# Performance work log

Hardware: AMD Instinct MI355X
Metric: run time of the kernel (lower is better)

## Reference

```python
import jax, jax.numpy as jnp
import numpy as np

DIM = 4096
N_HEADS = 32
HEAD_DIM = DIM // N_HEADS  # 128
BSZ = 2
SEQLEN = 2048


def setup_inputs() -> dict:
    key = jax.random.key(0)
    ks = jax.random.split(key, 8)
    x = jax.random.normal(ks[0], (BSZ, SEQLEN, DIM), dtype=jnp.float32)
    # rotary frequencies (LLaMA): theta = 10000^{-2i/d}, angle = pos * theta
    inv_freq = 1.0 / (10000.0 ** (np.arange(0, HEAD_DIM, 2, dtype=np.float32) / HEAD_DIM))
    angles = np.arange(SEQLEN, dtype=np.float32)[:, None] * inv_freq[None, :]  # [S, hd/2]
    freqs_cos = jnp.asarray(np.cos(angles))
    freqs_sin = jnp.asarray(np.sin(angles))
    # causal additive mask [1,1,S,S]
    neg = jnp.float32(-1e9)
    mask = jnp.where(jnp.tril(jnp.ones((SEQLEN, SEQLEN), dtype=bool)), 0.0, neg)[None, None]
    scale = 0.02
    wq = jax.random.normal(ks[1], (DIM, DIM), dtype=jnp.float32) * scale
    wk = jax.random.normal(ks[2], (DIM, DIM), dtype=jnp.float32) * scale
    wv = jax.random.normal(ks[3], (DIM, DIM), dtype=jnp.float32) * scale
    wo = jax.random.normal(ks[4], (DIM, DIM), dtype=jnp.float32) * scale
    return {"x": x, "start_pos": 0, "freqs_cos": freqs_cos, "freqs_sin": freqs_sin,
            "mask": mask, "wq": wq, "wk": wk, "wv": wv, "wo": wo}


def _apply_rotary(t, cos, sin):
    # t: [B,S,H,hd]; cos/sin: [S,hd/2] -> broadcast [1,S,1,hd/2]
    t = t.reshape(*t.shape[:-1], HEAD_DIM // 2, 2)
    t0, t1 = t[..., 0], t[..., 1]
    c = cos[None, :, None, :]
    s = sin[None, :, None, :]
    r0 = t0 * c - t1 * s
    r1 = t0 * s + t1 * c
    return jnp.stack([r0, r1], axis=-1).reshape(*t0.shape[:-1], HEAD_DIM)


def reference(x, start_pos, freqs_cos, freqs_sin, mask, wq, wk, wv, wo):
    bsz, seqlen, _ = x.shape
    # QKV projections (nn.Linear: y = x @ W.T; weights stored [out,in])
    xq = (x @ wq.T).reshape(bsz, seqlen, N_HEADS, HEAD_DIM)
    xk = (x @ wk.T).reshape(bsz, seqlen, N_HEADS, HEAD_DIM)
    xv = (x @ wv.T).reshape(bsz, seqlen, N_HEADS, HEAD_DIM)
    xq = _apply_rotary(xq, freqs_cos, freqs_sin)
    xk = _apply_rotary(xk, freqs_cos, freqs_sin)
    # [B,H,S,hd]
    q = xq.transpose(0, 2, 1, 3)
    k = xk.transpose(0, 2, 1, 3)
    v = xv.transpose(0, 2, 1, 3)
    scale = 1.0 / jnp.sqrt(jnp.float32(HEAD_DIM))
    scores = jnp.einsum('bhqd,bhkd->bhqk', q, k) * scale + mask
    probs = jax.nn.softmax(scores, axis=-1)
    out = jnp.einsum('bhqk,bhkd->bhqd', probs, v)  # [B,H,S,hd]
    out = out.transpose(0, 2, 1, 3).reshape(bsz, seqlen, DIM)
    return out @ wo.T
```

## Files before the change

kernel.cpp:

```cpp
#include <hip/hip_runtime.h>

typedef unsigned short ushort_t;
typedef unsigned int u32;
typedef short bf16x8 __attribute__((ext_vector_type(8)));
typedef float f32x4 __attribute__((ext_vector_type(4)));
typedef float f32x16 __attribute__((ext_vector_type(16)));
typedef u32 u32x4 __attribute__((ext_vector_type(4)));

__device__ __forceinline__ ushort_t f2bf(float f) {
  u32 u = __builtin_bit_cast(u32, f);
  u += 0x7FFFu + ((u >> 16) & 1u);
  return (ushort_t)(u >> 16);
}
__device__ __forceinline__ float bf2f(u32 bits16) {
  return __builtin_bit_cast(float, bits16 << 16);
}

__device__ __forceinline__ void cvt_body(const float* __restrict__ in,
                                         ushort_t* __restrict__ out, int i) {
  const float4 a = ((const float4*)in)[(size_t)i * 2];
  const float4 b = ((const float4*)in)[(size_t)i * 2 + 1];
  uint4 r;
  r.x = (u32)f2bf(a.x) | ((u32)f2bf(a.y) << 16);
  r.y = (u32)f2bf(a.z) | ((u32)f2bf(a.w) << 16);
  r.z = (u32)f2bf(b.x) | ((u32)f2bf(b.y) << 16);
  r.w = (u32)f2bf(b.z) | ((u32)f2bf(b.w) << 16);
  ((uint4*)out)[i] = r;
}

__device__ __forceinline__ void cvt_perm_body(const float* __restrict__ in,
                                              ushort_t* __restrict__ out, int i) {
  const int row = i >> 9, k8 = i & 511;
  const int q = row & 31;
  const int lrow = (row & ~31) | ((q < 16) ? (2 * q) : (2 * (q - 16) + 1));
  const float4 a = ((const float4*)in)[(size_t)lrow * 1024 + k8 * 2];
  const float4 b = ((const float4*)in)[(size_t)lrow * 1024 + k8 * 2 + 1];
  uint4 r;
  r.x = (u32)f2bf(a.x) | ((u32)f2bf(a.y) << 16);
  r.y = (u32)f2bf(a.z) | ((u32)f2bf(a.w) << 16);
  r.z = (u32)f2bf(b.x) | ((u32)f2bf(b.y) << 16);
  r.w = (u32)f2bf(b.z) | ((u32)f2bf(b.w) << 16);
  ((uint4*)out)[(size_t)row * 512 + k8] = r;
}

__global__ __launch_bounds__(256)
void cvt_kernel(const float* __restrict__ in, ushort_t* __restrict__ out) {
  cvt_body(in, out, blockIdx.x * 256 + threadIdx.x);
}

__global__ __launch_bounds__(256)
void cvt_perm_kernel(const float* __restrict__ in, ushort_t* __restrict__ out) {
  cvt_perm_body(in, out, blockIdx.x * 256 + threadIdx.x);
}

__global__ __launch_bounds__(256)
void cvt2_kernel(const float* __restrict__ i0, ushort_t* __restrict__ o0,
                 const float* __restrict__ i1, ushort_t* __restrict__ o1,
                 const float* __restrict__ fcos, const float* __restrict__ fsin,
                 float2* __restrict__ cst) {
  const int i = blockIdx.x * 256 + threadIdx.x;
  if (blockIdx.y == 0) {
    if (blockIdx.x < 512) cst[i] = make_float2(fcos[i], fsin[i]);
    cvt_body(i0, o0, i);
  } else {
    cvt_perm_body(i1, o1, i);
  }
}

template <int F32OUT, int ROPE>
__global__ __launch_bounds__(512, 2)
void gemm256(const ushort_t* __restrict__ A, const ushort_t* __restrict__ B,
             void* __restrict__ C, const float2* __restrict__ cst, float qsc) {
  constexpr int KD = 4096, ND = 4096;
  __shared__ ushort_t sA[2][2][128 * 64];
  __shared__ ushort_t sB[2][2][128 * 64];
  const int tid = threadIdx.x;
  const int lane = tid & 63, wave = tid >> 6;
  const int lq = lane & 15, g = lane >> 4;
  const int wm = wave >> 2, wn = wave & 3;
  const int id = blockIdx.x;
  const int swz = (id & 7) * 32 + (id >> 3);
  const int bm = (swz >> 4) * 256;
  const int bn = (swz & 15) * 256;
  const int csw = ((lane & 7) ^ (lane >> 3)) * 8;
  const int srow = lane >> 3;

  f32x4 acc[8][4];
#pragma unroll
  for (int m = 0; m < 8; ++m)
#pragma unroll
    for (int n = 0; n < 4; ++n) acc[m][n] = (f32x4)0.f;

#define STG(sbuf, G, rowb, t_, s_, h_)                                               \
  {                                                                                  \
    _Pragma("unroll") for (int i_ = 0; i_ < 2; ++i_) {                               \
      const int r0_ = wave * 16 + i_ * 8;                                            \
      const int tc_ = (t_) > 63 ? 63 : (t_);                                         \
      const ushort_t* src_ =                                                         \
          (G) + (size_t)((rowb) + (h_) * 128 + r0_ + srow) * KD + tc_ * 64 + csw;    \
      __builtin_amdgcn_global_load_lds(                                              \
          (const __attribute__((address_space(1))) u32*)src_,                        \
          (__attribute__((address_space(3))) u32*)&sbuf[s_][h_][r0_ * 64 + lane * 8],\
          16, 0, 0);                                                                 \
    }                                                                                \
  }
#define RD_A(S_, H_, mf_, kk_)                                                        \
  (*(const bf16x8*)&sA[S_][H_][(wm * 64 + (mf_) * 16 + lq) * 64 +                     \
                               ((((kk_) * 4 + g) ^ (lq & 7)) * 8)])
#define RD_B(S_, H_, nf_, kk_)                                                        \
  (*(const bf16x8*)&sB[S_][H_][(wn * 32 + (nf_) * 16 + lq) * 64 +                     \
                               ((((kk_) * 4 + g) ^ (lq & 7)) * 8)])
#define MM2(MB, B0R, B1R)                                                             \
  _Pragma("unroll") for (int mf = 0; mf < 4; ++mf)                                    \
    _Pragma("unroll") for (int nf = 0; nf < 2; ++nf)                                  \
      _Pragma("unroll") for (int kk = 0; kk < 2; ++kk) {                              \
        acc[(MB) + mf][nf] = __builtin_amdgcn_mfma_f32_16x16x32_bf16(                 \
            af[mf][kk], B0R[nf][kk], acc[(MB) + mf][nf], 0, 0, 0);                    \
        acc[(MB) + mf][2 + nf] = __builtin_amdgcn_mfma_f32_16x16x32_bf16(             \
            af[mf][kk], B1R[nf][kk], acc[(MB) + mf][2 + nf], 0, 0, 0);                \
      }

  STG(sA, A, bm, 0, 0, 0); STG(sA, A, bm, 0, 0, 1);
  STG(sB, B, bn, 0, 0, 0); STG(sB, B, bn, 0, 0, 1);
  asm volatile("s_waitcnt vmcnt(0)" ::: "memory");
  __builtin_amdgcn_s_barrier();
  __builtin_amdgcn_sched_barrier(0);

  bf16x8 af[4][2], b0[2][2], b1[2][2];

#define TILE(S_, T_)                                                                  \
  STG(sA, A, bm, (T_) + 1, (S_) ^ 1, 0);                                              \
  STG(sA, A, bm, (T_) + 1, (S_) ^ 1, 1);                                              \
  STG(sB, B, bn, (T_) + 1, (S_) ^ 1, 0);                                              \
  STG(sB, B, bn, (T_) + 1, (S_) ^ 1, 1);                                              \
  _Pragma("unroll") for (int mf = 0; mf < 4; ++mf)                                    \
    _Pragma("unroll") for (int kk = 0; kk < 2; ++kk)                                  \
      af[mf][kk] = RD_A(S_, 0, mf, kk);                                               \
  _Pragma("unroll") for (int nf = 0; nf < 2; ++nf)                                    \
    _Pragma("unroll") for (int kk = 0; kk < 2; ++kk) {                                \
      b0[nf][kk] = RD_B(S_, 0, nf, kk);                                               \
      b1[nf][kk] = RD_B(S_, 1, nf, kk);                                               \
    }                                                                                 \
  __builtin_amdgcn_s_setprio(1);                                                      \
  MM2(0, b0, b1);                                                                     \
  __builtin_amdgcn_s_setprio(0);                                                      \
  _Pragma("unroll") for (int mf = 0; mf < 4; ++mf)                                    \
    _Pragma("unroll") for (int kk = 0; kk < 2; ++kk)                                  \
      af[mf][kk] = RD_A(S_, 1, mf, kk);                                               \
  __builtin_amdgcn_s_setprio(1);                                                      \
  MM2(4, b0, b1);                                                                     \
  __builtin_amdgcn_s_setprio(0);                                                      \
  asm volatile("s_waitcnt vmcnt(0)" ::: "memory");                                    \
  __builtin_amdgcn_s_barrier();                                                       \
  __builtin_amdgcn_sched_barrier(0);

  for (int t = 0; t < 64; t += 2) {
    TILE(0, t)
    TILE(1, t + 1)
  }
#undef TILE
#undef STG
#undef RD_A
#undef RD_B
#undef MM2

  if (ROPE) {
    const int p = wn * 16 + lq;
#pragma unroll
    for (int m = 0; m < 8; ++m) {
      const int grow = bm + (m >> 2) * 128 + wm * 64 + (m & 3) * 16 + g * 4;
#pragma unroll
      for (int r = 0; r < 4; ++r) {
        const int row = grow + r;
        const float2 cs = cst[(size_t)(row & 2047) * 64 + p];
#pragma unroll
        for (int pr = 0; pr < 2; ++pr) {
          const float t0 = acc[m][pr * 2][r];
          const float t1 = acc[m][pr * 2 + 1][r];
          const int c0 = bn + pr * 128 + wn * 32 + lq;
          ((ushort_t*)C)[(size_t)row * ND + c0] =
              f2bf((t0 * cs.x - t1 * cs.y) * qsc);
          ((ushort_t*)C)[(size_t)row * ND + c0 + 16] =
              f2bf((t0 * cs.y + t1 * cs.x) * qsc);
        }
      }
    }
  } else {
#pragma unroll
    for (int m = 0; m < 8; ++m) {
      const int grow = bm + (m >> 2) * 128 + wm * 64 + (m & 3) * 16 + g * 4;
#pragma unroll
      for (int r = 0; r < 4; ++r) {
        const int row = grow + r;
#pragma unroll
        for (int n = 0; n < 4; ++n) {
          const int gcol = bn + (n >> 1) * 128 + wn * 32 + (n & 1) * 16 + lq;
          if (F32OUT)
            ((float*)C)[(size_t)row * ND + gcol] = acc[m][n][r];
          else
            ((ushort_t*)C)[(size_t)row * ND + gcol] = f2bf(acc[m][n][r]);
        }
      }
    }
  }
}

__global__ __launch_bounds__(256, 2)
void attn_kernel(const ushort_t* __restrict__ Q, const ushort_t* __restrict__ K,
                 const ushort_t* __restrict__ Vt, ushort_t* __restrict__ O) {
  __shared__ ushort_t sK[2][32 * 128];
  __shared__ ushort_t sV[2][128 * 32];
  __shared__ float sScr[4][32];

  const int lane = threadIdx.x & 63, wave = threadIdx.x >> 6;
  const int lq = lane & 31, hi = lane >> 5;
  const int bp = blockIdx.x;
  const int bh = bp >> 3, j = bp & 7;
  const int h = bh & 31, b = bh >> 5;
  const ushort_t* Kb_ = K + (size_t)(b * 2048) * 4096 + h * 128;
  const ushort_t* Vb_ = Vt + (size_t)(h * 128) * 4096 + b * 2048;

#define STAGE(buf, kt_)                                                              \
  {                                                                                  \
    const int kb_ = (kt_) * 32;                                                      \
    _Pragma("unroll")                                                                \
    for (int i_ = 0; i_ < 2; ++i_) {                                                 \
      const int c_ = wave + i_ * 4;                                                  \
      const int krow = c_ * 4 + (lane >> 4);                                         \
      const int kcol = (lane & 15) ^ (krow & 7);                                     \
      const ushort_t* ksrc = Kb_ + (size_t)(kb_ + krow) * 4096 + kcol * 8;           \
      __builtin_amdgcn_global_load_lds(                                              \
          (const __attribute__((address_space(1))) u32*)ksrc,                        \
          (__attribute__((address_space(3))) u32*)&sK[buf][c_ * 512 + lane * 8],     \
          16, 0, 0);                                                                 \
      const int sst = c_ * 64 + lane;                                                \
      const int dv = sst >> 2;                                                       \
      const int gl = (sst & 3) ^ ((sst >> 3) & 3);                                   \
      const ushort_t* vsrc = Vb_ + (size_t)dv * 4096 + kb_ + gl * 8;                 \
      __builtin_amdgcn_global_load_lds(                                              \
          (const __attribute__((address_space(1))) u32*)vsrc,                        \
          (__attribute__((address_space(3))) u32*)&sV[buf][sst * 8], 16, 0, 0);      \
    }                                                                                \
  }

  for (int ph = 0; ph < 2; ++ph) {
    const int qj = ph ? (15 - j) : j;
    const int qbase = qj * 128 + wave * 32;
    const int ntw = qj * 4 + wave + 1;
    const int ntmax = qj * 4 + 4;

    bf16x8 aq[8];
    const ushort_t* qrow = Q + (size_t)(b * 2048 + qbase + lq) * 4096 + h * 128 + hi * 8;
#pragma unroll
    for (int kf = 0; kf < 8; ++kf) aq[kf] = *(const bf16x8*)(qrow + kf * 16);

    f32x16 o[4];
#pragma unroll
    for (int dt = 0; dt < 4; ++dt) o[dt] = (f32x16)0.f;
    float m_run = -1e30f, l_run = 0.f;

    int cur = 0;
    STAGE(0, 0);
    __syncthreads();

    for (int kt = 0; kt < ntmax; ++kt) {
      if (kt + 1 < ntmax) STAGE(cur ^ 1, kt + 1);
      if (kt < ntw) {
        const int kb = kt * 32;
        f32x16 st = (f32x16)0.f;
#pragma unroll
        for (int kf = 0; kf < 8; ++kf) {
          const bf16x8 kfrag =
              *(const bf16x8*)&sK[cur][lq * 128 + (((kf * 2 + hi) ^ (lq & 7)) * 8)];
          st = __builtin_amdgcn_mfma_f32_32x32x16_bf16(kfrag, aq[kf], st, 0, 0, 0);
        }
        if (kt == ntw - 1) {
          const int q = qbase + lq;
#pragma unroll
          for (int r = 0; r < 16; ++r) {
            const int key = kb + (r & 3) + 8 * (r >> 2) + 4 * hi;
            if (key > q) st[r] = -1e30f;
          }
        }
        float tm = st[0];
#pragma unroll
        for (int r = 1; r < 16; ++r) tm = fmaxf(tm, st[r]);
        tm = fmaxf(tm, __shfl_xor(tm, 32));
        if (!__all(tm <= m_run + 8.f)) {
          const float mnew = fmaxf(m_run, tm);
          const float corr = __expf(m_run - mnew);
          m_run = mnew;
          l_run *= corr;
          if (hi == 0) sScr[wave][lq] = corr;
          float fr[16];
#pragma unroll
          for (int r = 0; r < 16; ++r)
            fr[r] = sScr[wave][(r & 3) + 8 * (r >> 2) + 4 * hi];
#pragma unroll
          for (int dt = 0; dt < 4; ++dt)
#pragma unroll
            for (int r = 0; r < 16; ++r) o[dt][r] *= fr[r];
        }
        float rs = 0.f;
#pragma unroll
        for (int r = 0; r < 16; ++r) { st[r] = __expf(st[r] - m_run); rs += st[r]; }
        rs += __shfl_xor(rs, 32);
        l_run += rs;
        u32 A_, B_, C_, D_, E_, F_, G_, H_;
#define CVTPK(d_, l_, h_) \
  asm("v_cvt_pk_bf16_f32 %0, %1, %2" : "=v"(d_) : "v"(l_), "v"(h_))
        CVTPK(A_, st[0], st[1]);  CVTPK(B_, st[4], st[5]);
        CVTPK(C_, st[2], st[3]);  CVTPK(D_, st[6], st[7]);
        CVTPK(E_, st[8], st[9]);  CVTPK(F_, st[12], st[13]);
        CVTPK(G_, st[10], st[11]); CVTPK(H_, st[14], st[15]);
#undef CVTPK
        asm volatile("v_permlane32_swap_b32 %0, %1" : "+v"(A_), "+v"(B_));
        asm volatile("v_permlane32_swap_b32 %0, %1" : "+v"(C_), "+v"(D_));
        asm volatile("v_permlane32_swap_b32 %0, %1" : "+v"(E_), "+v"(F_));
        asm volatile("v_permlane32_swap_b32 %0, %1" : "+v"(G_), "+v"(H_));
        const bf16x8 pa0 = __builtin_bit_cast(bf16x8, (u32x4){A_, C_, B_, D_});
        const bf16x8 pa1 = __builtin_bit_cast(bf16x8, (u32x4){E_, G_, F_, H_});
#pragma unroll
        for (int dt = 0; dt < 4; ++dt) {
          const int d0 = dt * 32 + lq;
          const int s0 = 4 * d0 + ((hi + 0) ^ ((d0 >> 1) & 3));
          const int s1 = 4 * d0 + ((hi + 2) ^ ((d0 >> 1) & 3));
          const bf16x8 vf0 = *(const bf16x8*)&sV[cur][s0 * 8];
          const bf16x8 vf1 = *(const bf16x8*)&sV[cur][s1 * 8];
          o[dt] = __builtin_amdgcn_mfma_f32_32x32x16_bf16(pa0, vf0, o[dt], 0, 0, 0);
          o[dt] = __builtin_amdgcn_mfma_f32_32x32x16_bf16(pa1, vf1, o[dt], 0, 0, 0);
        }
      }
      __syncthreads();
      cur ^= 1;
    }

    if (hi == 0) sScr[wave][lq] = 1.f / l_run;
    __syncthreads();
    const size_t obase = (size_t)(b * 2048 + qbase) * 4096 + h * 128;
#pragma unroll
    for (int r = 0; r < 16; ++r) {
      const int qr = (r & 3) + 8 * (r >> 2) + 4 * hi;
      const float f = sScr[wave][qr];
#pragma unroll
      for (int dt = 0; dt < 4; ++dt)
        O[obase + (size_t)qr * 4096 + dt * 32 + lq] = f2bf(o[dt][r] * f);
    }
    __syncthreads();
  }
#undef STAGE
}

extern "C" void kernel_launch(void* const* d_in, const int* in_sizes, int n_in,
                              void* d_out, int out_size, void* d_ws, size_t ws_size,
                              hipStream_t stream) {
  const float* x = (const float*)d_in[0];
  const float* fcos = (const float*)d_in[2];
  const float* fsin = (const float*)d_in[3];
  const float* wq = (const float*)d_in[5];
  const float* wk = (const float*)d_in[6];
  const float* wv = (const float*)d_in[7];
  const float* wo = (const float*)d_in[8];
  float* out = (float*)d_out;
  char* ws = (char*)d_ws;
  const size_t MB32 = 33554432;
  ushort_t* xb = (ushort_t*)(ws);
  ushort_t* wb = (ushort_t*)(ws + MB32);
  ushort_t* Qb = (ushort_t*)(ws + 2 * MB32);
  ushort_t* Kb = (ushort_t*)(ws + 3 * MB32);
  ushort_t* Vt = (ushort_t*)(ws + 4 * MB32);
  ushort_t* Ob = xb;
  float2* cst = (float2*)d_out;

  const dim3 cb(256);
  const dim3 cg(8192);
  const dim3 gb(512);
  const dim3 gg(256);
  const float QSC = 0.08838834764831845f;

  hipLaunchKernelGGL(cvt2_kernel, dim3(8192, 2), cb, 0, stream, x, xb, wq, wb,
                     fcos, fsin, cst);
  hipLaunchKernelGGL((gemm256<0, 1>), gg, gb, 0, stream, xb, wb, (void*)Qb, cst, QSC);
  hipLaunchKernelGGL(cvt_perm_kernel, cg, cb, 0, stream, wk, wb);
  hipLaunchKernelGGL((gemm256<0, 1>), gg, gb, 0, stream, xb, wb, (void*)Kb, cst, 1.f);
  hipLaunchKernelGGL(cvt_kernel, cg, cb, 0, stream, wv, wb);
  hipLaunchKernelGGL((gemm256<0, 0>), gg, gb, 0, stream, wb, xb, (void*)Vt, cst, 1.f);
  hipLaunchKernelGGL(attn_kernel, dim3(512), cb, 0, stream, Qb, Kb, Vt, Ob);
  hipLaunchKernelGGL(cvt_kernel, cg, cb, 0, stream, wo, wb);
  hipLaunchKernelGGL((gemm256<1, 0>), gg, gb, 0, stream, Ob, wb, (void*)out, cst, 1.f);
}
```

Before: 664.9 us.

## Restructure GEMM mainloop into quadrant-staged pipeline with deeper prefetch

The GEMM main loop drops the two-stage pattern, where each iteration issues all loads for the next tile and then waits on vmcnt(0). It now splits work into four MFMA quadrants, each paired with its own LDS reads and global-to-LDS loads, and prefetches half-tiles two steps ahead with a partial vmcnt(6) wait. The goal is to hide global-load latency behind MFMA work and avoid the full drain at every tile. In exchange it adds many more workgroup barriers per tile, and the buffer-reuse ordering is intricate, so it risks LDS hazards and barrier stalls.

```diff
diff --git a/kernel.cpp b/kernel.cpp
--- a/kernel.cpp
+++ b/kernel.cpp
@@ -110,49 +110,64 @@
 #define RD_B(S_, H_, nf_, kk_)                                                        \
   (*(const bf16x8*)&sB[S_][H_][(wn * 32 + (nf_) * 16 + lq) * 64 +                     \
                                ((((kk_) * 4 + g) ^ (lq & 7)) * 8)])
-#define MM2(MB, B0R, B1R)                                                             \
+#define MMQ(MB, NB, BR)                                                               \
   _Pragma("unroll") for (int mf = 0; mf < 4; ++mf)                                    \
     _Pragma("unroll") for (int nf = 0; nf < 2; ++nf)                                  \
-      _Pragma("unroll") for (int kk = 0; kk < 2; ++kk) {                              \
-        acc[(MB) + mf][nf] = __builtin_amdgcn_mfma_f32_16x16x32_bf16(                 \
-            af[mf][kk], B0R[nf][kk], acc[(MB) + mf][nf], 0, 0, 0);                    \
-        acc[(MB) + mf][2 + nf] = __builtin_amdgcn_mfma_f32_16x16x32_bf16(             \
-            af[mf][kk], B1R[nf][kk], acc[(MB) + mf][2 + nf], 0, 0, 0);                \
-      }
+      _Pragma("unroll") for (int kk = 0; kk < 2; ++kk)                                \
+        acc[(MB) + mf][(NB) + nf] = __builtin_amdgcn_mfma_f32_16x16x32_bf16(          \
+            af[mf][kk], BR[nf][kk], acc[(MB) + mf][(NB) + nf], 0, 0, 0)
 
   STG(sA, A, bm, 0, 0, 0); STG(sA, A, bm, 0, 0, 1);
   STG(sB, B, bn, 0, 0, 0); STG(sB, B, bn, 0, 0, 1);
-  asm volatile("s_waitcnt vmcnt(0)" ::: "memory");
+  STG(sA, A, bm, 1, 1, 0); STG(sA, A, bm, 1, 1, 1);
+  STG(sB, B, bn, 1, 1, 1);
+  asm volatile("s_waitcnt vmcnt(6)" ::: "memory");
   __builtin_amdgcn_s_barrier();
-  __builtin_amdgcn_sched_barrier(0);
 
   bf16x8 af[4][2], b0[2][2], b1[2][2];
 
 #define TILE(S_, T_)                                                                  \
-  STG(sA, A, bm, (T_) + 1, (S_) ^ 1, 0);                                              \
-  STG(sA, A, bm, (T_) + 1, (S_) ^ 1, 1);                                              \
-  STG(sB, B, bn, (T_) + 1, (S_) ^ 1, 0);                                              \
-  STG(sB, B, bn, (T_) + 1, (S_) ^ 1, 1);                                              \
+                      \
   _Pragma("unroll") for (int mf = 0; mf < 4; ++mf)                                    \
     _Pragma("unroll") for (int kk = 0; kk < 2; ++kk)                                  \
       af[mf][kk] = RD_A(S_, 0, mf, kk);                                               \
   _Pragma("unroll") for (int nf = 0; nf < 2; ++nf)                                    \
-    _Pragma("unroll") for (int kk = 0; kk < 2; ++kk) {                                \
+    _Pragma("unroll") for (int kk = 0; kk < 2; ++kk)                                  \
       b0[nf][kk] = RD_B(S_, 0, nf, kk);                                               \
+  STG(sB, B, bn, (T_) + 1, (S_) ^ 1, 0);                                              \
+  __builtin_amdgcn_s_barrier();                                                       \
+  __builtin_amdgcn_s_setprio(1);                                                      \
+  MMQ(0, 0, b0);                                                                      \
+  __builtin_amdgcn_s_setprio(0);                                                      \
+  __builtin_amdgcn_s_barrier();                                                       \
+                                                \
+  _Pragma("unroll") for (int nf = 0; nf < 2; ++nf)                                    \
+    _Pragma("unroll") for (int kk = 0; kk < 2; ++kk)                                  \
       b1[nf][kk] = RD_B(S_, 1, nf, kk);                                               \
-    }                                                                                 \
+  __builtin_amdgcn_s_barrier();                                                       \
   __builtin_amdgcn_s_setprio(1);                                                      \
-  MM2(0, b0, b1);                                                                     \
+  MMQ(0, 2, b1);                                                                      \
   __builtin_amdgcn_s_setprio(0);                                                      \
+  __builtin_amdgcn_s_barrier();                                                       \
+                              \
   _Pragma("unroll") for (int mf = 0; mf < 4; ++mf)                                    \
     _Pragma("unroll") for (int kk = 0; kk < 2; ++kk)                                  \
       af[mf][kk] = RD_A(S_, 1, mf, kk);                                               \
+  STG(sA, A, bm, (T_) + 2, S_, 0);                                                    \
+  __builtin_amdgcn_s_barrier();                                                       \
   __builtin_amdgcn_s_setprio(1);                                                      \
-  MM2(4, b0, b1);                                                                     \
+  MMQ(4, 2, b1);                                                                      \
   __builtin_amdgcn_s_setprio(0);                                                      \
-  asm volatile("s_waitcnt vmcnt(0)" ::: "memory");                                    \
-  __builtin_amdgcn_s_barrier();                                                       \
-  __builtin_amdgcn_sched_barrier(0);
+  __builtin_amdgcn_s_barrier();                                                       \
+                     \
+  STG(sA, A, bm, (T_) + 2, S_, 1);                                                    \
+  STG(sB, B, bn, (T_) + 2, S_, 1);                                                    \
+  asm volatile("s_waitcnt vmcnt(6)" ::: "memory");                                    \
+  __builtin_amdgcn_s_barrier();                                                       \
+  __builtin_amdgcn_s_setprio(1);                                                      \
+  MMQ(4, 0, b0);                                                                      \
+  __builtin_amdgcn_s_setprio(0);                                                      \
+  __builtin_amdgcn_s_barrier();
 
   for (int t = 0; t < 64; t += 2) {
     TILE(0, t)
@@ -162,7 +177,7 @@
 #undef STG
 #undef RD_A
 #undef RD_B
-#undef MM2
+#undef MMQ
 
   if (ROPE) {
     const int p = wn * 16 + lq;
```

After: 677.2 us. Within noise of the previous version (+1.8%).

## Fold weight conversions into GEMM and attention launches as extra blocks

Applied to the files above, without the earlier changes.

Removes the standalone fp32->bf16 weight conversion kernels and folds each into the preceding GEMM or attention launch as extra blocks. Those blocks convert the next weight matrix while the compute blocks run. Buffers are rotated (Vt is reused as temporary weight storage for the K projection) so the conversion does not overwrite operands still in use. This saves launch gaps and lets memory-bound conversion overlap compute, at the cost of extra grid blocks competing for CUs and a tighter buffer-aliasing scheme.

```diff
diff --git a/kernel.cpp b/kernel.cpp
--- a/kernel.cpp
+++ b/kernel.cpp
@@ -44,16 +44,6 @@
 }
 
 __global__ __launch_bounds__(256)
-void cvt_kernel(const float* __restrict__ in, ushort_t* __restrict__ out) {
-  cvt_body(in, out, blockIdx.x * 256 + threadIdx.x);
-}
-
-__global__ __launch_bounds__(256)
-void cvt_perm_kernel(const float* __restrict__ in, ushort_t* __restrict__ out) {
-  cvt_perm_body(in, out, blockIdx.x * 256 + threadIdx.x);
-}
-
-__global__ __launch_bounds__(256)
 void cvt2_kernel(const float* __restrict__ i0, ushort_t* __restrict__ o0,
                  const float* __restrict__ i1, ushort_t* __restrict__ o1,
                  const float* __restrict__ fcos, const float* __restrict__ fsin,
@@ -67,18 +57,29 @@
   }
 }
 
-template <int F32OUT, int ROPE>
+template <int F32OUT, int ROPE, int CVT>
 __global__ __launch_bounds__(512, 2)
 void gemm256(const ushort_t* __restrict__ A, const ushort_t* __restrict__ B,
-             void* __restrict__ C, const float2* __restrict__ cst, float qsc) {
+             void* __restrict__ C, const float2* __restrict__ cst, float qsc,
+             const float* __restrict__ csrc, ushort_t* __restrict__ cdst) {
   constexpr int KD = 4096, ND = 4096;
   __shared__ ushort_t sA[2][2][128 * 64];
   __shared__ ushort_t sB[2][2][128 * 64];
   const int tid = threadIdx.x;
+  const int id = blockIdx.x;
+  if (CVT && id >= 256) {
+    const int cb_ = id - 256;
+#pragma unroll 2
+    for (int it = 0; it < 8; ++it) {
+      const int i = it * 262144 + cb_ * 512 + tid;
+      if (CVT == 1) cvt_perm_body(csrc, cdst, i);
+      else cvt_body(csrc, cdst, i);
+    }
+    return;
+  }
   const int lane = tid & 63, wave = tid >> 6;
   const int lq = lane & 15, g = lane >> 4;
   const int wm = wave >> 2, wn = wave & 3;
-  const int id = blockIdx.x;
   const int swz = (id & 7) * 32 + (id >> 3);
   const int bm = (swz >> 4) * 256;
   const int bn = (swz & 15) * 256;
@@ -207,14 +208,23 @@
 
 __global__ __launch_bounds__(256, 2)
 void attn_kernel(const ushort_t* __restrict__ Q, const ushort_t* __restrict__ K,
-                 const ushort_t* __restrict__ Vt, ushort_t* __restrict__ O) {
+                 const ushort_t* __restrict__ Vt, ushort_t* __restrict__ O,
+                 const float* __restrict__ csrc, ushort_t* __restrict__ cdst) {
   __shared__ ushort_t sK[2][32 * 128];
   __shared__ ushort_t sV[2][128 * 32];
   __shared__ float sScr[4][32];
 
+  const int bp = blockIdx.x;
+  if (bp >= 512) {
+    const int cb_ = bp - 512;
+#pragma unroll 2
+    for (int it = 0; it < 16; ++it)
+      cvt_body(csrc, cdst, it * 131072 + cb_ * 256 + threadIdx.x);
+    return;
+  }
+
   const int lane = threadIdx.x & 63, wave = threadIdx.x >> 6;
   const int lq = lane & 31, hi = lane >> 5;
-  const int bp = blockIdx.x;
   const int bh = bp >> 3, j = bp & 7;
   const int h = bh & 31, b = bh >> 5;
   const ushort_t* Kb_ = K + (size_t)(b * 2048) * 4096 + h * 128;
@@ -373,19 +383,18 @@
   float2* cst = (float2*)d_out;
 
   const dim3 cb(256);
-  const dim3 cg(8192);
   const dim3 gb(512);
-  const dim3 gg(256);
   const float QSC = 0.08838834764831845f;
 
   hipLaunchKernelGGL(cvt2_kernel, dim3(8192, 2), cb, 0, stream, x, xb, wq, wb,
                      fcos, fsin, cst);
-  hipLaunchKernelGGL((gemm256<0, 1>), gg, gb, 0, stream, xb, wb, (void*)Qb, cst, QSC);
-  hipLaunchKernelGGL(cvt_perm_kernel, cg, cb, 0, stream, wk, wb);
-  hipLaunchKernelGGL((gemm256<0, 1>), gg, gb, 0, stream, xb, wb, (void*)Kb, cst, 1.f);
-  hipLaunchKernelGGL(cvt_kernel, cg, cb, 0, stream, wv, wb);
-  hipLaunchKernelGGL((gemm256<0, 0>), gg, gb, 0, stream, wb, xb, (void*)Vt, cst, 1.f);
-  hipLaunchKernelGGL(attn_kernel, dim3(512), cb, 0, stream, Qb, Kb, Vt, Ob);
-  hipLaunchKernelGGL(cvt_kernel, cg, cb, 0, stream, wo, wb);
-  hipLaunchKernelGGL((gemm256<1, 0>), gg, gb, 0, stream, Ob, wb, (void*)out, cst, 1.f);
-}
+  hipLaunchKernelGGL((gemm256<0, 1, 1>), dim3(768), gb, 0, stream, xb, wb,
+                     (void*)Qb, cst, QSC, wk, Vt);
+  hipLaunchKernelGGL((gemm256<0, 1, 2>), dim3(768), gb, 0, stream, xb, Vt,
+                     (void*)Kb, cst, 1.f, wv, wb);
+  hipLaunchKernelGGL((gemm256<0, 0, 0>), dim3(256), gb, 0, stream, wb, xb,
+                     (void*)Vt, cst, 1.f, nullptr, nullptr);
+  hipLaunchKernelGGL(attn_kernel, dim3(1024), cb, 0, stream, Qb, Kb, Vt, Ob, wo, wb);
+  hipLaunchKernelGGL((gemm256<1, 0, 0>), dim3(256), gb, 0, stream, Ob, wb,
+                     (void*)out, cst, 1.f, nullptr, nullptr);
+}
```

Measured after the change: 657.8 us (median of 3 runs). No clear change (-1.1%).
